# Optimization experiments

Hardware: AMD Instinct MI355X
Metric: run time of the kernel (lower is better)

Reference implementation:

```python
import jax, jax.numpy as jnp
import numpy as np

B, LI, LT = 1, 2048, 256
HID, HEADS, HD = 3072, 24, 128
MLP = 4 * HID  # 12288
EPS = 1e-6


def setup_inputs() -> dict:
    key = jax.random.key(0)
    ks = jax.random.split(key, 12)
    n = lambda k, s, sc=1.0: jax.random.normal(k, s, dtype=jnp.float32) * sc
    # RoPE tables, interleaved-pair layout over head_dim
    theta = 10000.0 ** (-jnp.arange(0, HD, 2, dtype=jnp.float32) / HD)  # [HD/2]
    ang = jnp.arange(LI, dtype=jnp.float32)[:, None] * theta[None, :]   # [LI, HD/2]
    freqs_cos = jnp.repeat(jnp.cos(ang), 2, axis=-1)  # [LI, HD]
    freqs_sin = jnp.repeat(jnp.sin(ang), 2, axis=-1)
    return {
        "img": n(ks[0], (B, LI, HID)),
        "txt": n(ks[1], (B, LT, HID)),
        "vec": n(ks[2], (B, HID)),
        "freqs_cos": freqs_cos,
        "freqs_sin": freqs_sin,
        "w1": n(ks[3], (3 * HID + MLP, HID), 0.02),
        "b1": jnp.zeros((3 * HID + MLP,), jnp.float32),
        "w2": n(ks[4], (HID, HID + MLP), 0.02),
        "b2": jnp.zeros((HID,), jnp.float32),
        "q_norm_w": jnp.ones((HD,), jnp.float32),
        "k_norm_w": jnp.ones((HD,), jnp.float32),
        "mod_w": n(ks[5], (3 * HID, HID), 0.02),
        "mod_b": jnp.zeros((3 * HID,), jnp.float32),
        "txt_len": LT,
    }


def _layernorm(x):  # no affine, eps=1e-6
    mu = x.mean(-1, keepdims=True)
    var = ((x - mu) ** 2).mean(-1, keepdims=True)
    return (x - mu) * jax.lax.rsqrt(var + EPS)


def _rmsnorm(x, w):  # per-head-dim RMSNorm with affine weight
    ms = (x * x).mean(-1, keepdims=True)
    return x * jax.lax.rsqrt(ms + EPS) * w


def _rope(x, cos, sin):  # x: [B,L,H,D]; interleaved complex rotation
    xr = x.reshape(*x.shape[:-1], HD // 2, 2)
    rot = jnp.stack([-xr[..., 1], xr[..., 0]], axis=-1).reshape(x.shape)
    return x * cos[None, :, None, :] + rot * sin[None, :, None, :]


def reference(img, txt, vec, freqs_cos, freqs_sin, w1, b1, w2, b2,
              q_norm_w, k_norm_w, mod_w, mod_b, txt_len):
    H = img.shape[-1]
    Li = img.shape[1]
    # modulation: SiLU(vec) @ W -> shift, scale, gate
    mod = jax.nn.silu(vec) @ mod_w.T + mod_b           # [B, 3H]
    shift, scale, gate = jnp.split(mod, 3, axis=-1)
    modulate = lambda x: x * (1.0 + scale[:, None, :]) + shift[:, None, :]
    img_mod = modulate(_layernorm(img))
    txt_mod = modulate(_layernorm(txt))
    x_mod = jnp.concatenate([img_mod, txt_mod], axis=1)  # [B,S,H]
    Bb, S = x_mod.shape[0], x_mod.shape[1]
    # fused QKV projection (slices of linear1)
    qkv = x_mod @ w1[: 3 * H].T + b1[: 3 * H]
    q, k, v = [t.reshape(Bb, S, HEADS, HD) for t in jnp.split(qkv, 3, axis=-1)]
    q = _rmsnorm(q, q_norm_w)
    k = _rmsnorm(k, k_norm_w)
    # RoPE only on the img portion of the sequence
    q = jnp.concatenate([_rope(q[:, :Li], freqs_cos, freqs_sin), q[:, Li:]], axis=1)
    k = jnp.concatenate([_rope(k[:, :Li], freqs_cos, freqs_sin), k[:, Li:]], axis=1)
    # full (non-causal) attention over img+txt tokens
    logits = jnp.einsum('bqhd,bkhd->bhqk', q, k) * (HD ** -0.5)
    probs = jax.nn.softmax(logits, axis=-1)
    attn = jnp.einsum('bhqk,bkhd->bqhd', probs, v).reshape(Bb, S, H)
    # MLP branch (linear1 mlp slice) with gelu-tanh, then fused linear2
    mlp = jax.nn.gelu(x_mod @ w1[3 * H:].T + b1[3 * H:], approximate=True)
    out = jnp.concatenate([attn, mlp], axis=-1) @ w2.T + b2  # [B,S,H]
    img_out = img + gate[:, None, :] * out[:, :-txt_len]
    txt_out = txt + gate[:, None, :] * out[:, -txt_len:]
    return img_out, txt_out
```

## Files before the change

kernel.cpp:

```cpp
#include <hip/hip_runtime.h>
#include <hip/hip_bf16.h>

#define DI __device__ __forceinline__

typedef __attribute__((ext_vector_type(8))) short bf8;
typedef __attribute__((ext_vector_type(4))) float f4;
typedef __attribute__((ext_vector_type(8))) unsigned short us8;

#define LI    2048
#define LT    256
#define SEQ   2304
#define HID   3072
#define NHEAD 24
#define HD    128
#define N1    21504
#define QKVW  9216
#define N2CAT 15360

DI unsigned short f2bf(float f) {
  union { float f; unsigned u; } v; v.f = f;
  unsigned r = v.u + 0x7FFFu + ((v.u >> 16) & 1u);
  return (unsigned short)(r >> 16);
}
DI float bf2f(unsigned short h) {
  union { unsigned u; float f; } v; v.u = ((unsigned)h) << 16;
  return v.f;
}

DI void gload16(const void* g, void* l) {
  __builtin_amdgcn_global_load_lds(
      (const __attribute__((address_space(1))) void*)g,
      (__attribute__((address_space(3))) void*)l, 16, 0, 0);
}

DI f4 mfma16(bf8 a, bf8 b, f4 c) {
  return __builtin_amdgcn_mfma_f32_16x16x32_bf16(a, b, c, 0, 0, 0);
}

__global__ void k_mod(const float* __restrict__ vec, const float* __restrict__ mw,
                      const float* __restrict__ mb, float* __restrict__ mod) {
  int row = blockIdx.x * 4 + (threadIdx.x >> 6);
  int lane = threadIdx.x & 63;
  const float4* wr = (const float4*)(mw + (size_t)row * HID);
  const float4* vv = (const float4*)vec;
  float s = 0.f;
  for (int i = lane; i < HID / 4; i += 64) {
    float4 w4 = wr[i], x4 = vv[i];
    s += (x4.x / (1.f + __expf(-x4.x))) * w4.x;
    s += (x4.y / (1.f + __expf(-x4.y))) * w4.y;
    s += (x4.z / (1.f + __expf(-x4.z))) * w4.z;
    s += (x4.w / (1.f + __expf(-x4.w))) * w4.w;
  }
#pragma unroll
  for (int m = 32; m; m >>= 1) s += __shfl_xor(s, m);
  if (lane == 0) mod[row] = s + mb[row];
}

__global__ void k_lnmod(const float* __restrict__ img, const float* __restrict__ txt,
                        const float* __restrict__ mod, unsigned short* __restrict__ xmod,
                        const float* __restrict__ w1, unsigned short* __restrict__ w1b) {
  int t = blockIdx.x;
  if (t >= SEQ) {
    int cb = t - SEQ;
    const int n4 = N1 * HID / 4;
    for (int i = cb * 256 + threadIdx.x; i < n4; i += 1024 * 256) {
      float4 f = ((const float4*)w1)[i];
      ushort4 o;
      o.x = f2bf(f.x); o.y = f2bf(f.y); o.z = f2bf(f.z); o.w = f2bf(f.w);
      ((ushort4*)w1b)[i] = o;
    }
    return;
  }
  const float* x = (t < LI) ? (img + (size_t)t * HID) : (txt + (size_t)(t - LI) * HID);
  const float4* x4 = (const float4*)x;
  float4 v[3];
  float s = 0.f, ss = 0.f;
#pragma unroll
  for (int j = 0; j < 3; ++j) {
    v[j] = x4[threadIdx.x + j * 256];
    s  += v[j].x + v[j].y + v[j].z + v[j].w;
    ss += v[j].x * v[j].x + v[j].y * v[j].y + v[j].z * v[j].z + v[j].w * v[j].w;
  }
#pragma unroll
  for (int m = 32; m; m >>= 1) { s += __shfl_xor(s, m); ss += __shfl_xor(ss, m); }
  __shared__ float red[8];
  int wv = threadIdx.x >> 6;
  if ((threadIdx.x & 63) == 0) { red[wv] = s; red[4 + wv] = ss; }
  __syncthreads();
  s = red[0] + red[1] + red[2] + red[3];
  ss = red[4] + red[5] + red[6] + red[7];
  float mu = s * (1.f / HID);
  float var = ss * (1.f / HID) - mu * mu;
  float inv = rsqrtf(var + 1e-6f);
  const float* shift = mod;
  const float* scale = mod + HID;
#pragma unroll
  for (int j = 0; j < 3; ++j) {
    int i = threadIdx.x + j * 256;
    int c = i * 4;
    ushort4 o;
    o.x = f2bf((v[j].x - mu) * inv * (1.f + scale[c + 0]) + shift[c + 0]);
    o.y = f2bf((v[j].y - mu) * inv * (1.f + scale[c + 1]) + shift[c + 1]);
    o.z = f2bf((v[j].z - mu) * inv * (1.f + scale[c + 2]) + shift[c + 2]);
    o.w = f2bf((v[j].w - mu) * inv * (1.f + scale[c + 3]) + shift[c + 3]);
    ((ushort4*)xmod)[(size_t)t * (HID / 4) + i] = o;
  }
}

#define BAR()    asm volatile("s_barrier" ::: "memory")
#define VMCNT6() asm volatile("s_waitcnt vmcnt(6)" ::: "memory")
#define VMCNT4() asm volatile("s_waitcnt vmcnt(4)" ::: "memory")
#define VMCNT2() asm volatile("s_waitcnt vmcnt(2)" ::: "memory")
#define VMCNT0() asm volatile("s_waitcnt vmcnt(0)" ::: "memory")
#define LGKM0()  do { asm volatile("s_waitcnt lgkmcnt(0)" ::: "memory"); \
                      __builtin_amdgcn_sched_barrier(0); } while (0)

__global__ __launch_bounds__(512, 2) void k_gemm1(const unsigned short* __restrict__ xmod,
    const unsigned short* __restrict__ w1b, const float* __restrict__ b1,
    unsigned short* __restrict__ qkv, unsigned short* __restrict__ amlp) {
  __shared__ unsigned short As[2][256 * 64];
  __shared__ unsigned short Bs[2][256 * 64];
  const int K = HID;
  const int NT = K / 64;
  int tid = threadIdx.x, lane = tid & 63, wid = tid >> 6;
  int wr = wid >> 2, wc = wid & 3;

  int b = blockIdx.x;
  const int Q = 756 / 8, R = 756 % 8;
  int xcd = b & 7, idx = b >> 3;
  int wg = (xcd < R ? xcd * (Q + 1) : R * (Q + 1) + (xcd - R) * Q) + idx;
  int bm = wg % 9, bn = wg / 9;

  const unsigned short* Ag = xmod + (size_t)bm * 256 * K;
  const unsigned short* Bg = w1b + (size_t)bn * 256 * K;

  int sgran = (lane & 7) ^ ((lane >> 3) & 7);
  int srow = wid * 16 + (lane >> 3);

#define STAGE_A(bufi, t, hh) do { \
    gload16(Ag + (size_t)((hh)*128 + srow) * K + (t)*64 + sgran*8, \
            &As[bufi][((hh)*128 + wid*16) * 64]); \
    gload16(Ag + (size_t)((hh)*128 + 8 + srow) * K + (t)*64 + sgran*8, \
            &As[bufi][((hh)*128 + wid*16 + 8) * 64]); \
  } while (0)
#define STAGE_B(bufi, t, hh) do { \
    gload16(Bg + (size_t)((hh)*128 + srow) * K + (t)*64 + sgran*8, \
            &Bs[bufi][((hh)*128 + wid*16) * 64]); \
    gload16(Bg + (size_t)((hh)*128 + 8 + srow) * K + (t)*64 + sgran*8, \
            &Bs[bufi][((hh)*128 + wid*16 + 8) * 64]); \
  } while (0)

  int rA = wr * 128 + (lane & 15);
  int rB = wc * 64 + (lane & 15);
  int qq = lane >> 4, l7 = lane & 7;

  f4 acc[8][4];
#pragma unroll
  for (int m = 0; m < 8; ++m)
#pragma unroll
    for (int n = 0; n < 4; ++n) acc[m][n] = (f4){0.f, 0.f, 0.f, 0.f};
  bf8 aL[4][2], aH[4][2], bL[2][2], bH[2][2];

#define RD(buf, r, s) (*(const bf8*)&buf[(r) * 64 + ((((s)*4 + qq) ^ l7) << 3)])

#define GROUP(C, tn, tn2) do { \
    _Pragma("unroll") for (int m = 0; m < 4; ++m) \
      _Pragma("unroll") for (int s = 0; s < 2; ++s) aL[m][s] = RD(As[C], rA + m*16, s); \
    _Pragma("unroll") for (int n = 0; n < 2; ++n) \
      _Pragma("unroll") for (int s = 0; s < 2; ++s) bL[n][s] = RD(Bs[C], rB + n*16, s); \
    STAGE_A(1-(C), tn, 1); STAGE_B(1-(C), tn, 0); STAGE_B(1-(C), tn, 1); \
    LGKM0(); \
    __builtin_amdgcn_s_setprio(1); \
    _Pragma("unroll") for (int m = 0; m < 4; ++m) \
      _Pragma("unroll") for (int n = 0; n < 2; ++n) \
        _Pragma("unroll") for (int s = 0; s < 2; ++s) \
          acc[m][n] = mfma16(aL[m][s], bL[n][s], acc[m][n]); \
    __builtin_amdgcn_s_setprio(0); \
    _Pragma("unroll") for (int n = 0; n < 2; ++n) \
      _Pragma("unroll") for (int s = 0; s < 2; ++s) bH[n][s] = RD(Bs[C], rB + (n+2)*16, s); \
    LGKM0(); \
    __builtin_amdgcn_s_setprio(1); \
    _Pragma("unroll") for (int m = 0; m < 4; ++m) \
      _Pragma("unroll") for (int n = 0; n < 2; ++n) \
        _Pragma("unroll") for (int s = 0; s < 2; ++s) \
          acc[m][n+2] = mfma16(aL[m][s], bH[n][s], acc[m][n+2]); \
    __builtin_amdgcn_s_setprio(0); \
    _Pragma("unroll") for (int m = 0; m < 4; ++m) \
      _Pragma("unroll") for (int s = 0; s < 2; ++s) aH[m][s] = RD(As[C], rA + (m+4)*16, s); \
    LGKM0(); \
    BAR(); \
    __builtin_amdgcn_s_setprio(1); \
    _Pragma("unroll") for (int m = 0; m < 4; ++m) \
      _Pragma("unroll") for (int n = 0; n < 2; ++n) \
        _Pragma("unroll") for (int s = 0; s < 2; ++s) \
          acc[m+4][n+2] = mfma16(aH[m][s], bH[n][s], acc[m+4][n+2]); \
    __builtin_amdgcn_s_setprio(0); \
    STAGE_A(C, tn2, 0); \
    __builtin_amdgcn_s_setprio(1); \
    _Pragma("unroll") for (int m = 0; m < 4; ++m) \
      _Pragma("unroll") for (int n = 0; n < 2; ++n) \
        _Pragma("unroll") for (int s = 0; s < 2; ++s) \
          acc[m+4][n] = mfma16(aH[m][s], bL[n][s], acc[m+4][n]); \
    __builtin_amdgcn_s_setprio(0); \
    VMCNT2(); \
    BAR(); \
  } while (0)

  STAGE_A(0, 0, 0); STAGE_A(0, 0, 1); STAGE_B(0, 0, 0); STAGE_B(0, 0, 1);
  STAGE_A(1, 1, 0);
  VMCNT2();
  BAR();

  for (int i = 0; i < NT / 2; ++i) {
    int t0 = 2 * i;
    int n1 = t0 + 2; if (n1 > NT - 1) n1 = NT - 1;
    int n2 = t0 + 3; if (n2 > NT - 1) n2 = NT - 1;
    GROUP(0, t0 + 1, n1);
    GROUP(1, n1, n2);
  }
  VMCNT0();

  int r0 = bm * 256 + wr * 128 + ((lane >> 4) << 2);
  int c0 = bn * 256 + wc * 64 + (lane & 15);
  bool isqkv = (bn * 256) < QKVW;
#pragma unroll
  for (int m = 0; m < 8; ++m) {
#pragma unroll
    for (int n = 0; n < 4; ++n) {
      int col = c0 + n * 16;
      float bias = b1[col];
#pragma unroll
      for (int j = 0; j < 4; ++j) {
        int row = r0 + m * 16 + j;
        float v = acc[m][n][j] + bias;
        if (isqkv) {
          qkv[(size_t)row * QKVW + col] = f2bf(v);
        } else {
          float u = 0.7978845608f * (v + 0.044715f * v * v * v);
          float g = v / (1.f + __expf(-2.f * u));
          amlp[(size_t)row * N2CAT + (col - 6144)] = f2bf(g);
        }
      }
    }
  }
#undef STAGE_A
#undef STAGE_B
#undef RD
#undef GROUP
}

__global__ __launch_bounds__(512, 2) void k_gemm2(const unsigned short* __restrict__ amlp,
    const unsigned short* __restrict__ w2b, const float* __restrict__ b2,
    const float* __restrict__ img, const float* __restrict__ txt,
    const float* __restrict__ gate, float* __restrict__ out) {
  __shared__ unsigned short As[3][256 * 64];
  __shared__ unsigned short Bs[3][128 * 64];
  const int K = N2CAT;
  const int NT = K / 64;
  int tid = threadIdx.x, lane = tid & 63, wid = tid >> 6;
  int wr = wid >> 1, wc = wid & 1;

  int b = blockIdx.x;
  int bsw = (b & 7) * 27 + (b >> 3);
  int bm = bsw % 9, bn = bsw / 9;

  const unsigned short* Ag = amlp + (size_t)bm * 256 * K;
  const unsigned short* Bg = w2b + (size_t)bn * 128 * K;

  int sgran = (lane & 7) ^ ((lane >> 3) & 7);
  int srow = wid * 16 + (lane >> 3);

#define STAGE2_A(bufi, t, hh) do { \
    gload16(Ag + (size_t)((hh)*128 + srow) * K + (t)*64 + sgran*8, \
            &As[bufi][((hh)*128 + wid*16) * 64]); \
    gload16(Ag + (size_t)((hh)*128 + 8 + srow) * K + (t)*64 + sgran*8, \
            &As[bufi][((hh)*128 + wid*16 + 8) * 64]); \
  } while (0)
#define STAGE2_B(bufi, t) do { \
    gload16(Bg + (size_t)(srow) * K + (t)*64 + sgran*8, \
            &Bs[bufi][(wid*16) * 64]); \
    gload16(Bg + (size_t)(8 + srow) * K + (t)*64 + sgran*8, \
            &Bs[bufi][(wid*16 + 8) * 64]); \
  } while (0)

  int rA = wr * 64 + (lane & 15);
  int rB = wc * 64 + (lane & 15);
  int qq = lane >> 4, l7 = lane & 7;

  f4 acc[4][4];
#pragma unroll
  for (int m = 0; m < 4; ++m)
#pragma unroll
    for (int n = 0; n < 4; ++n) acc[m][n] = (f4){0.f, 0.f, 0.f, 0.f};
  bf8 aL[2][2], aH[2][2], bL[2][2], bH[2][2];

#define RD2(buf, r, s) (*(const bf8*)&buf[(r) * 64 + ((((s)*4 + qq) ^ l7) << 3)])

#define GROUP2(C, SB, t, full) do { \
    _Pragma("unroll") for (int m = 0; m < 2; ++m) \
      _Pragma("unroll") for (int s = 0; s < 2; ++s) aL[m][s] = RD2(As[C], rA + m*16, s); \
    _Pragma("unroll") for (int n = 0; n < 2; ++n) \
      _Pragma("unroll") for (int s = 0; s < 2; ++s) bL[n][s] = RD2(Bs[C], rB + n*16, s); \
    if (full) STAGE2_A(SB, (t) + 2, 0); \
    LGKM0(); \
    __builtin_amdgcn_s_setprio(1); \
    _Pragma("unroll") for (int m = 0; m < 2; ++m) \
      _Pragma("unroll") for (int n = 0; n < 2; ++n) \
        _Pragma("unroll") for (int s = 0; s < 2; ++s) \
          acc[m][n] = mfma16(aL[m][s], bL[n][s], acc[m][n]); \
    __builtin_amdgcn_s_setprio(0); \
    BAR(); \
    _Pragma("unroll") for (int n = 0; n < 2; ++n) \
      _Pragma("unroll") for (int s = 0; s < 2; ++s) bH[n][s] = RD2(Bs[C], rB + (n+2)*16, s); \
    if (full) STAGE2_A(SB, (t) + 2, 1); \
    LGKM0(); \
    __builtin_amdgcn_s_setprio(1); \
    _Pragma("unroll") for (int m = 0; m < 2; ++m) \
      _Pragma("unroll") for (int n = 0; n < 2; ++n) \
        _Pragma("unroll") for (int s = 0; s < 2; ++s) \
          acc[m][n+2] = mfma16(aL[m][s], bH[n][s], acc[m][n+2]); \
    __builtin_amdgcn_s_setprio(0); \
    BAR(); \
    _Pragma("unroll") for (int m = 0; m < 2; ++m) \
      _Pragma("unroll") for (int s = 0; s < 2; ++s) aH[m][s] = RD2(As[C], rA + (m+2)*16, s); \
    if (full) STAGE2_B(SB, (t) + 2); \
    LGKM0(); \
    __builtin_amdgcn_s_setprio(1); \
    _Pragma("unroll") for (int m = 0; m < 2; ++m) \
      _Pragma("unroll") for (int n = 0; n < 2; ++n) \
        _Pragma("unroll") for (int s = 0; s < 2; ++s) \
          acc[m+2][n+2] = mfma16(aH[m][s], bH[n][s], acc[m+2][n+2]); \
    __builtin_amdgcn_s_setprio(0); \
    BAR(); \
    __builtin_amdgcn_s_setprio(1); \
    _Pragma("unroll") for (int m = 0; m < 2; ++m) \
      _Pragma("unroll") for (int n = 0; n < 2; ++n) \
        _Pragma("unroll") for (int s = 0; s < 2; ++s) \
          acc[m+2][n] = mfma16(aH[m][s], bL[n][s], acc[m+2][n]); \
    __builtin_amdgcn_s_setprio(0); \
    if (full) { VMCNT6(); } else { VMCNT0(); } \
    BAR(); \
  } while (0)

  STAGE2_A(0, 0, 0); STAGE2_A(0, 0, 1); STAGE2_B(0, 0);
  STAGE2_A(1, 1, 0); STAGE2_A(1, 1, 1); STAGE2_B(1, 1);
  VMCNT6();
  BAR();

  for (int i = 0; i < NT / 3; ++i) {
    int t = 3 * i;
    GROUP2(0, 2, t,     (t + 2) < NT);
    GROUP2(1, 0, t + 1, (t + 3) < NT);
    GROUP2(2, 1, t + 2, (t + 4) < NT);
  }
  VMCNT0();

  int r0 = bm * 256 + wr * 64 + ((lane >> 4) << 2);
  int c0 = bn * 128 + wc * 64 + (lane & 15);
#pragma unroll
  for (int m = 0; m < 4; ++m) {
#pragma unroll
    for (int n = 0; n < 4; ++n) {
      int col = c0 + n * 16;
      float bias = b2[col];
      float gt = gate[col];
#pragma unroll
      for (int j = 0; j < 4; ++j) {
        int row = r0 + m * 16 + j;
        float v = acc[m][n][j] + bias;
        float res = (row < LI) ? img[(size_t)row * HID + col]
                               : txt[(size_t)(row - LI) * HID + col];
        out[(size_t)row * HID + col] = res + gt * v;
      }
    }
  }
#undef STAGE2_A
#undef STAGE2_B
#undef RD2
#undef GROUP2
}

__global__ void k_qkvt(unsigned short* __restrict__ qkv, const float* __restrict__ qw,
                       const float* __restrict__ kw, const float* __restrict__ fcos,
                       const float* __restrict__ fsin, unsigned short* __restrict__ vt) {
  int b = blockIdx.x;
  int tid = threadIdx.x;
  __shared__ unsigned short tile[64 * 65];
  if (b < 13824) {
    int gw = (b * 256 + tid) >> 6;
    int lane = tid & 63;
    int token = gw / NHEAD, head = gw - token * NHEAD;
    bool dorope = token < LI;
    float c = 1.f, sn = 0.f;
    if (dorope) { c = fcos[token * HD + 2 * lane]; sn = fsin[token * HD + 2 * lane]; }
#pragma unroll
    for (int qk = 0; qk < 2; ++qk) {
      unsigned short* p = qkv + (size_t)token * QKVW + qk * HID + head * HD;
      unsigned u = ((const unsigned*)p)[lane];
      float x0 = bf2f((unsigned short)(u & 0xffff));
      float x1 = bf2f((unsigned short)(u >> 16));
      float ss = x0 * x0 + x1 * x1;
#pragma unroll
      for (int m2 = 32; m2; m2 >>= 1) ss += __shfl_xor(ss, m2);
      float inv = rsqrtf(ss * (1.f / HD) + 1e-6f);
      const float* w = qk ? kw : qw;
      float y0 = x0 * inv * w[2 * lane];
      float y1 = x1 * inv * w[2 * lane + 1];
      if (dorope) { float r0 = y0 * c - y1 * sn; float r1 = y1 * c + y0 * sn; y0 = r0; y1 = r1; }
      ((unsigned*)p)[lane] = ((unsigned)f2bf(y0)) | (((unsigned)f2bf(y1)) << 16);
    }
  } else {
    int bb = b - 13824;
    int h = bb / 72; int rem = bb - h * 72; int tt = rem >> 1; int dd = rem & 1;
    int t0 = tt * 64, d0 = dd * 64;
#pragma unroll
    for (int j = 0; j < 2; ++j) {
      int idx = j * 256 + tid;
      int row = idx >> 3, s = idx & 7;
      us8 vv = *(const us8*)(qkv + (size_t)(t0 + row) * QKVW + 2 * HID + h * HD + d0 + s * 8);
#pragma unroll
      for (int i = 0; i < 8; ++i) tile[row * 65 + s * 8 + i] = vv[i];
    }
    __syncthreads();
#pragma unroll
    for (int j = 0; j < 2; ++j) {
      int idx = j * 256 + tid;
      int dr = idx >> 3, sl = idx & 7;
      us8 o;
#pragma unroll
      for (int i = 0; i < 8; ++i) o[i] = tile[(sl * 8 + i) * 65 + dr];
      *(us8*)(vt + (size_t)(h * HD + d0 + dr) * SEQ + t0 + sl * 8) = o;
    }
  }
}

__global__ __launch_bounds__(512, 4) void k_attn(const unsigned short* __restrict__ qkv,
                                                 const unsigned short* __restrict__ vt,
                                                 unsigned short* __restrict__ amlp,
                                                 const float* __restrict__ w2,
                                                 unsigned short* __restrict__ w2b) {
  int b = blockIdx.x;
  int tid = threadIdx.x;
  if (b >= 432) {
    int cb = b - 432;
    const int n4 = HID * N2CAT / 4;
    for (int i = cb * 512 + tid; i < n4; i += 768 * 512) {
      float4 f = ((const float4*)w2)[i];
      ushort4 o;
      o.x = f2bf(f.x); o.y = f2bf(f.y); o.z = f2bf(f.z); o.w = f2bf(f.w);
      ((ushort4*)w2b)[i] = o;
    }
    return;
  }
  __shared__ unsigned short S[40960];
  unsigned short* Ks = S;
  unsigned short* Vs = S + 16384;
  unsigned short* Ps = S + 32768;

  int bsw = (b & 7) * 54 + (b >> 3);
  int head = bsw / 18, qt = bsw - head * 18;
  int lane = tid & 63, wv = tid >> 6;
  int qbase = qt * 128;

#define STAGEK(dst, t) do { \
    int rl_ = tid >> 4, sl_ = tid & 15, sg_ = sl_ ^ (rl_ & 7); \
    const unsigned short* kg_ = qkv + HID + (size_t)((t) * 64 + rl_) * QKVW + head * HD + sg_ * 8; \
    gload16(kg_, &(dst)[tid * 8]); \
    gload16(kg_ + (size_t)32 * QKVW, &(dst)[(512 + tid) * 8]); \
  } while (0)
#define STAGEV(dst, t) do { \
    int rl_ = tid >> 3, sl_ = tid & 7, sg_ = sl_ ^ (rl_ & 7); \
    const unsigned short* vg_ = vt + (size_t)(head * HD + rl_) * SEQ + (t) * 64 + sg_ * 8; \
    gload16(vg_, &(dst)[tid * 8]); \
    gload16(vg_ + (size_t)64 * SEQ, &(dst)[(512 + tid) * 8]); \
  } while (0)

  bf8 qf[4];
  {
    const unsigned short* qp =
        qkv + (size_t)(qbase + wv * 16 + (lane & 15)) * QKVW + head * HD + (lane >> 4) * 8;
#pragma unroll
    for (int kk = 0; kk < 4; ++kk) qf[kk] = *(const bf8*)(qp + kk * 32);
  }
  STAGEK(Ks, 0); STAGEV(Vs, 0);
  STAGEK(Ks + 8192, 1); STAGEV(Vs + 8192, 1);
  VMCNT4();
  BAR();

  float mrun[4], lrun[4];
  f4 oacc[8];
#pragma unroll
  for (int j = 0; j < 4; ++j) { mrun[j] = -1e30f; lrun[j] = 0.f; }
#pragma unroll
  for (int n = 0; n < 8; ++n) oacc[n] = (f4){0.f, 0.f, 0.f, 0.f};

  for (int kt = 0; kt < SEQ / 64; ++kt) {
    int cur = kt & 1;
    const unsigned short* Kc = Ks + cur * 8192;
    const unsigned short* Vc = Vs + cur * 8192;
    f4 sacc[4];
#pragma unroll
    for (int n = 0; n < 4; ++n) sacc[n] = (f4){0.f, 0.f, 0.f, 0.f};
#pragma unroll
    for (int kk = 0; kk < 4; ++kk) {
#pragma unroll
      for (int n = 0; n < 4; ++n) {
        int row = n * 16 + (lane & 15);
        int col = (kk * 32 + ((lane >> 4) * 8)) ^ ((lane & 7) << 3);
        bf8 kf = *(const bf8*)&Kc[row * 128 + col];
        sacc[n] = mfma16(qf[kk], kf, sacc[n]);
      }
    }
    const float SC = 0.08838834764831845f;
    float mj[4];
#pragma unroll
    for (int j = 0; j < 4; ++j)
      mj[j] = fmaxf(fmaxf(sacc[0][j], sacc[1][j]), fmaxf(sacc[2][j], sacc[3][j]));
#pragma unroll
    for (int j = 0; j < 4; ++j) {
#pragma unroll
      for (int mk = 8; mk; mk >>= 1) mj[j] = fmaxf(mj[j], __shfl_xor(mj[j], mk));
    }
    float resc[4], psum[4];
#pragma unroll
    for (int j = 0; j < 4; ++j) {
      float nm = fmaxf(mrun[j], mj[j] * SC);
      resc[j] = __expf(mrun[j] - nm);
      mrun[j] = nm;
      psum[j] = 0.f;
    }
#pragma unroll
    for (int n = 0; n < 4; ++n) {
#pragma unroll
      for (int j = 0; j < 4; ++j) {
        float p = __expf(sacc[n][j] * SC - mrun[j]);
        psum[j] += p;
        int row = wv * 16 + ((lane >> 4) << 2) + j;
        int col = (n * 16 + (lane & 15)) ^ ((row & 7) << 3);
        Ps[row * 64 + col] = f2bf(p);
      }
    }
#pragma unroll
    for (int j = 0; j < 4; ++j) {
#pragma unroll
      for (int mk = 8; mk; mk >>= 1) psum[j] += __shfl_xor(psum[j], mk);
      lrun[j] = lrun[j] * resc[j] + psum[j];
    }
#pragma unroll
    for (int n = 0; n < 8; ++n) {
#pragma unroll
      for (int j = 0; j < 4; ++j) oacc[n][j] *= resc[j];
    }
#pragma unroll
    for (int kk = 0; kk < 2; ++kk) {
      int prow = wv * 16 + (lane & 15);
      int pcol = (kk * 32 + ((lane >> 4) * 8)) ^ ((lane & 7) << 3);
      bf8 pa = *(const bf8*)&Ps[prow * 64 + pcol];
#pragma unroll
      for (int n = 0; n < 8; ++n) {
        int vrow = n * 16 + (lane & 15);
        int vcol = (kk * 32 + ((lane >> 4) * 8)) ^ ((vrow & 7) << 3);
        bf8 vf = *(const bf8*)&Vc[vrow * 64 + vcol];
        oacc[n] = mfma16(pa, vf, oacc[n]);
      }
    }
    BAR();
    if (kt + 2 < SEQ / 64) {
      STAGEK(Ks + cur * 8192, kt + 2);
      STAGEV(Vs + cur * 8192, kt + 2);
      VMCNT4();
    } else {
      VMCNT0();
    }
    BAR();
  }
#undef STAGEK
#undef STAGEV

#pragma unroll
  for (int j = 0; j < 4; ++j) {
    float invl = 1.f / lrun[j];
    int row = qbase + wv * 16 + ((lane >> 4) << 2) + j;
#pragma unroll
    for (int n = 0; n < 8; ++n) {
      int col = head * HD + n * 16 + (lane & 15);
      amlp[(size_t)row * N2CAT + col] = f2bf(oacc[n][j] * invl);
    }
  }
}

extern "C" void kernel_launch(void* const* d_in, const int* in_sizes, int n_in,
                              void* d_out, int out_size, void* d_ws, size_t ws_size,
                              hipStream_t stream) {
  (void)in_sizes; (void)n_in; (void)out_size; (void)ws_size;
  const float* img  = (const float*)d_in[0];
  const float* txt  = (const float*)d_in[1];
  const float* vec  = (const float*)d_in[2];
  const float* fcos = (const float*)d_in[3];
  const float* fsin = (const float*)d_in[4];
  const float* w1   = (const float*)d_in[5];
  const float* b1   = (const float*)d_in[6];
  const float* w2   = (const float*)d_in[7];
  const float* b2   = (const float*)d_in[8];
  const float* qnw  = (const float*)d_in[9];
  const float* knw  = (const float*)d_in[10];
  const float* mw   = (const float*)d_in[11];
  const float* mb   = (const float*)d_in[12];
  float* out = (float*)d_out;

  char* ws = (char*)d_ws;
  float*          mod  = (float*)(ws);
  unsigned short* xmod = (unsigned short*)(ws + 40960);
  unsigned short* w1b  = (unsigned short*)(ws + 14196736);
  unsigned short* qkv  = (unsigned short*)(ws + 146317312);
  unsigned short* amlp = (unsigned short*)(ws + 188784640);
  unsigned short* vtb  = xmod;
  unsigned short* w2b  = w1b;

  k_mod<<<QKVW / 4, 256, 0, stream>>>(vec, mw, mb, mod);
  k_lnmod<<<SEQ + 1024, 256, 0, stream>>>(img, txt, mod, xmod, w1, w1b);
  k_gemm1<<<756, 512, 0, stream>>>(xmod, w1b, b1, qkv, amlp);
  k_qkvt<<<13824 + 1728, 256, 0, stream>>>(qkv, qnw, knw, fcos, fsin, vtb);
  k_attn<<<432 + 768, 512, 0, stream>>>(qkv, vtb, amlp, w2, w2b);
  k_gemm2<<<216, 512, 0, stream>>>(amlp, w2b, b2, img, txt, mod + 2 * HID, out);
}
```

Before: 874.0 us.

## Fuse Q/K RMSNorm and RoPE into the QKV GEMM epilogue

Moves the per-head RMSNorm and rotary embedding for Q and K into the epilogue of the first GEMM. Per-row sums of squares are reduced across lanes with shuffles and across the two waves that share a head through shared memory, and pair rotation uses a lane xor shuffle. The standalone normalisation pass only does the V transpose now, which removes a full read-modify-write of Q and K in global memory. In exchange the GEMM epilogue gains extra barriers, register pressure and scattered cos/sin loads.

```diff
diff --git a/kernel.cpp b/kernel.cpp
--- a/kernel.cpp
+++ b/kernel.cpp
@@ -117,7 +117,9 @@
 
 __global__ __launch_bounds__(512, 2) void k_gemm1(const unsigned short* __restrict__ xmod,
     const unsigned short* __restrict__ w1b, const float* __restrict__ b1,
-    unsigned short* __restrict__ qkv, unsigned short* __restrict__ amlp) {
+    unsigned short* __restrict__ qkv, unsigned short* __restrict__ amlp,
+    const float* __restrict__ qnw, const float* __restrict__ knw,
+    const float* __restrict__ fcos, const float* __restrict__ fsin) {
   __shared__ unsigned short As[2][256 * 64];
   __shared__ unsigned short Bs[2][256 * 64];
   const int K = HID;
@@ -222,23 +224,80 @@
 
   int r0 = bm * 256 + wr * 128 + ((lane >> 4) << 2);
   int c0 = bn * 256 + wc * 64 + (lane & 15);
-  bool isqkv = (bn * 256) < QKVW;
-#pragma unroll
-  for (int m = 0; m < 8; ++m) {
+  if (bn < 24) {
+    const float* wqk = (bn < 12) ? qnw : knw;
+    bool dorope = (bm < 8);
 #pragma unroll
     for (int n = 0; n < 4; ++n) {
-      int col = c0 + n * 16;
-      float bias = b1[col];
+      float bias = b1[c0 + n * 16];
+#pragma unroll
+      for (int m = 0; m < 8; ++m)
+#pragma unroll
+        for (int j = 0; j < 4; ++j) acc[m][n][j] += bias;
+    }
+    float ssv[8][4];
+#pragma unroll
+    for (int m = 0; m < 8; ++m)
 #pragma unroll
       for (int j = 0; j < 4; ++j) {
+        float s = 0.f;
+#pragma unroll
+        for (int n = 0; n < 4; ++n) s += acc[m][n][j] * acc[m][n][j];
+#pragma unroll
+        for (int mk = 8; mk; mk >>= 1) s += __shfl_xor(s, mk);
+        ssv[m][j] = s;
+      }
+    float* sred = (float*)&As[0][0];
+    BAR();
+    if ((lane & 15) == 0) {
+      int g = lane >> 4;
+#pragma unroll
+      for (int m = 0; m < 8; ++m)
+#pragma unroll
+        for (int j = 0; j < 4; ++j)
+          sred[wid * 128 + m * 16 + g * 4 + j] = ssv[m][j];
+    }
+    BAR();
+    int dbase = (wc & 1) * 64 + (lane & 15);
+#pragma unroll
+    for (int m = 0; m < 8; ++m) {
+#pragma unroll
+      for (int j = 0; j < 4; ++j) {
+        float tot = ssv[m][j] + sred[(wid ^ 1) * 128 + m * 16 + (lane >> 4) * 4 + j];
+        float inv = rsqrtf(tot * (1.f / HD) + 1e-6f);
         int row = r0 + m * 16 + j;
-        float v = acc[m][n][j] + bias;
-        if (isqkv) {
-          qkv[(size_t)row * QKVW + col] = f2bf(v);
-        } else {
-          float u = 0.7978845608f * (v + 0.044715f * v * v * v);
-          float g = v / (1.f + __expf(-2.f * u));
-          amlp[(size_t)row * N2CAT + (col - 6144)] = f2bf(g);
+#pragma unroll
+        for (int n = 0; n < 4; ++n) {
+          int d = dbase + n * 16;
+          float y = acc[m][n][j] * inv * wqk[d];
+          float yp = __shfl_xor(y, 1);
+          if (dorope) {
+            float cc = fcos[row * HD + d], sn = fsin[row * HD + d];
+            y = (d & 1) ? (y * cc + yp * sn) : (y * cc - yp * sn);
+          }
+          qkv[(size_t)row * QKVW + (c0 + n * 16)] = f2bf(y);
+        }
+      }
+    }
+  } else {
+    bool isv = (bn < 36);
+#pragma unroll
+    for (int m = 0; m < 8; ++m) {
+#pragma unroll
+      for (int n = 0; n < 4; ++n) {
+        int col = c0 + n * 16;
+        float bias = b1[col];
+#pragma unroll
+        for (int j = 0; j < 4; ++j) {
+          int row = r0 + m * 16 + j;
+          float v = acc[m][n][j] + bias;
+          if (isv) {
+            qkv[(size_t)row * QKVW + col] = f2bf(v);
+          } else {
+            float u = 0.7978845608f * (v + 0.044715f * v * v * v);
+            float g = v / (1.f + __expf(-2.f * u));
+            amlp[(size_t)row * N2CAT + (col - 6144)] = f2bf(g);
+          }
         }
       }
     }
@@ -380,57 +439,29 @@
 #undef GROUP2
 }
 
-__global__ void k_qkvt(unsigned short* __restrict__ qkv, const float* __restrict__ qw,
-                       const float* __restrict__ kw, const float* __restrict__ fcos,
-                       const float* __restrict__ fsin, unsigned short* __restrict__ vt) {
+__global__ void k_vt(const unsigned short* __restrict__ qkv, unsigned short* __restrict__ vt) {
   int b = blockIdx.x;
   int tid = threadIdx.x;
   __shared__ unsigned short tile[64 * 65];
-  if (b < 13824) {
-    int gw = (b * 256 + tid) >> 6;
-    int lane = tid & 63;
-    int token = gw / NHEAD, head = gw - token * NHEAD;
-    bool dorope = token < LI;
-    float c = 1.f, sn = 0.f;
-    if (dorope) { c = fcos[token * HD + 2 * lane]; sn = fsin[token * HD + 2 * lane]; }
-#pragma unroll
-    for (int qk = 0; qk < 2; ++qk) {
-      unsigned short* p = qkv + (size_t)token * QKVW + qk * HID + head * HD;
-      unsigned u = ((const unsigned*)p)[lane];
-      float x0 = bf2f((unsigned short)(u & 0xffff));
-      float x1 = bf2f((unsigned short)(u >> 16));
-      float ss = x0 * x0 + x1 * x1;
-#pragma unroll
-      for (int m2 = 32; m2; m2 >>= 1) ss += __shfl_xor(ss, m2);
-      float inv = rsqrtf(ss * (1.f / HD) + 1e-6f);
-      const float* w = qk ? kw : qw;
-      float y0 = x0 * inv * w[2 * lane];
-      float y1 = x1 * inv * w[2 * lane + 1];
-      if (dorope) { float r0 = y0 * c - y1 * sn; float r1 = y1 * c + y0 * sn; y0 = r0; y1 = r1; }
-      ((unsigned*)p)[lane] = ((unsigned)f2bf(y0)) | (((unsigned)f2bf(y1)) << 16);
-    }
-  } else {
-    int bb = b - 13824;
-    int h = bb / 72; int rem = bb - h * 72; int tt = rem >> 1; int dd = rem & 1;
-    int t0 = tt * 64, d0 = dd * 64;
-#pragma unroll
-    for (int j = 0; j < 2; ++j) {
-      int idx = j * 256 + tid;
-      int row = idx >> 3, s = idx & 7;
-      us8 vv = *(const us8*)(qkv + (size_t)(t0 + row) * QKVW + 2 * HID + h * HD + d0 + s * 8);
-#pragma unroll
-      for (int i = 0; i < 8; ++i) tile[row * 65 + s * 8 + i] = vv[i];
-    }
-    __syncthreads();
-#pragma unroll
-    for (int j = 0; j < 2; ++j) {
-      int idx = j * 256 + tid;
-      int dr = idx >> 3, sl = idx & 7;
-      us8 o;
-#pragma unroll
-      for (int i = 0; i < 8; ++i) o[i] = tile[(sl * 8 + i) * 65 + dr];
-      *(us8*)(vt + (size_t)(h * HD + d0 + dr) * SEQ + t0 + sl * 8) = o;
-    }
+  int h = b / 72; int rem = b - h * 72; int tt = rem >> 1; int dd = rem & 1;
+  int t0 = tt * 64, d0 = dd * 64;
+#pragma unroll
+  for (int j = 0; j < 2; ++j) {
+    int idx = j * 256 + tid;
+    int row = idx >> 3, s = idx & 7;
+    us8 vv = *(const us8*)(qkv + (size_t)(t0 + row) * QKVW + 2 * HID + h * HD + d0 + s * 8);
+#pragma unroll
+    for (int i = 0; i < 8; ++i) tile[row * 65 + s * 8 + i] = vv[i];
+  }
+  __syncthreads();
+#pragma unroll
+  for (int j = 0; j < 2; ++j) {
+    int idx = j * 256 + tid;
+    int dr = idx >> 3, sl = idx & 7;
+    us8 o;
+#pragma unroll
+    for (int i = 0; i < 8; ++i) o[i] = tile[(sl * 8 + i) * 65 + dr];
+    *(us8*)(vt + (size_t)(h * HD + d0 + dr) * SEQ + t0 + sl * 8) = o;
   }
 }
 
@@ -619,8 +650,8 @@
 
   k_mod<<<QKVW / 4, 256, 0, stream>>>(vec, mw, mb, mod);
   k_lnmod<<<SEQ + 1024, 256, 0, stream>>>(img, txt, mod, xmod, w1, w1b);
-  k_gemm1<<<756, 512, 0, stream>>>(xmod, w1b, b1, qkv, amlp);
-  k_qkvt<<<13824 + 1728, 256, 0, stream>>>(qkv, qnw, knw, fcos, fsin, vtb);
+  k_gemm1<<<756, 512, 0, stream>>>(xmod, w1b, b1, qkv, amlp, qnw, knw, fcos, fsin);
+  k_vt<<<NHEAD * 36 * 2, 256, 0, stream>>>(qkv, vtb);
   k_attn<<<432 + 768, 512, 0, stream>>>(qkv, vtb, amlp, w2, w2b);
   k_gemm2<<<216, 512, 0, stream>>>(amlp, w2b, b2, img, txt, mod + 2 * HID, out);
 }
```

Result: slower. 956.6 us (+9.5%).
